# Kernel optimization log

Measured on AMD Instinct MI355X. Metric: run time of the kernel, lower is better.

## Reference

```python
import jax, jax.numpy as jnp
import numpy as np

DIM = 2            # dimension along which stripes are dropped (1=time, 2=freq)
DROP_WIDTH = 64    # max stripe width
STRIPES_NUM = 2    # stripes per sample


def setup_inputs() -> dict:
    key = jax.random.key(0)
    k1, k2, k3 = jax.random.split(key, 3)
    x = jax.random.normal(k1, (64, 2048, 512), dtype=jnp.float32)
    u_dist = jax.random.uniform(k2, (64, STRIPES_NUM), dtype=jnp.float32)
    u_bgn = jax.random.uniform(k3, (64, STRIPES_NUM), dtype=jnp.float32)
    return {"x": x, "u_dist": u_dist, "u_bgn": u_bgn}


def _keep_mask(u_dist, u_bgn, total_width):
    # distance ~ randint(0, drop_width); bgn ~ randint(0, total_width - distance)
    distance = jnp.floor(u_dist * DROP_WIDTH).astype(jnp.int32)          # [B, S]
    bgn = jnp.floor(u_bgn * (total_width - distance)).astype(jnp.int32)  # [B, S]
    idx = jnp.arange(total_width, dtype=jnp.int32)                        # [W]
    in_stripe = (idx[None, None, :] >= bgn[:, :, None]) & (
        idx[None, None, :] < (bgn + distance)[:, :, None]
    )  # [B, S, W]
    return ~jnp.any(in_stripe, axis=1)  # [B, W] True where values are kept


def reference(x, u_dist, u_bgn):
    total_width = x.shape[DIM]
    keep = _keep_mask(u_dist, u_bgn, total_width)  # [B, W]
    if DIM == 1:
        keep = keep[:, :, None]  # broadcast over freq bins
    else:
        keep = keep[:, None, :]  # broadcast over time steps
    return x * keep.astype(x.dtype)
```

## Files before the change

### kernel.cpp

```cpp
#include <hip/hip_runtime.h>


__global__ void DropStripes_kernel(const float4* __restrict__ x,
                                   const float* __restrict__ u_dist,
                                   const float* __restrict__ u_bgn,
                                   float4* __restrict__ out,
                                   int n4) {
    constexpr int W4 = 512 / 4;
    int idx = blockIdx.x * blockDim.x + threadIdx.x;
    int stride = gridDim.x * blockDim.x;
    for (int i = idx; i < n4; i += stride) {
        int b  = i >> 18;
        int c0 = (i & (W4 - 1)) << 2;

        float ud0 = u_dist[2 * b];
        float ud1 = u_dist[2 * b + 1];
        float ub0 = u_bgn[2 * b];
        float ub1 = u_bgn[2 * b + 1];

        int dist0 = (int)floorf(ud0 * 64.0f);
        int dist1 = (int)floorf(ud1 * 64.0f);
        int bgn0  = (int)floorf(ub0 * (float)(512 - dist0));
        int bgn1  = (int)floorf(ub1 * (float)(512 - dist1));
        int end0  = bgn0 + dist0;
        int end1  = bgn1 + dist1;

        float4 v = x[i];
        float* vp = reinterpret_cast<float*>(&v);
        #pragma unroll
        for (int j = 0; j < 4; ++j) {
            int c = c0 + j;
            bool drop = (c >= bgn0 && c < end0) || (c >= bgn1 && c < end1);
            vp[j] = drop ? 0.0f : vp[j];
        }
        out[i] = v;
    }
}

extern "C" void kernel_launch(void* const* d_in, const int* in_sizes, int n_in,
                              void* d_out, int out_size, void* d_ws, size_t ws_size,
                              hipStream_t stream) {
    const float* x      = (const float*)d_in[0];
    const float* u_dist = (const float*)d_in[1];
    const float* u_bgn  = (const float*)d_in[2];
    float* out          = (float*)d_out;

    int n4 = out_size / 4;
    int block = 256;
    int grid = 8192;
    DropStripes_kernel<<<grid, block, 0, stream>>>(
        (const float4*)x, u_dist, u_bgn, (float4*)out, n4);
}
```

Before: 102.3 us.

## Assign blocks per batch and hoist stripe mask out of unrolled loop

Each block now handles a contiguous chunk inside one batch. The per-batch stripe bounds and the per-thread column mask are computed once instead of on every grid-stride iteration, and the fixed 8-iteration loop is fully unrolled so several loads can be in flight per thread. This removes repeated scalar loads and index math from a memory-bound streaming kernel. Shapes are now hard-coded, and because the mask is applied by multiplication, NaN or Inf inputs inside a stripe produce NaN instead of zero.

```diff
diff --git a/kernel.cpp b/kernel.cpp
--- a/kernel.cpp
+++ b/kernel.cpp
@@ -1,38 +1,52 @@
 #include <hip/hip_runtime.h>
 
 
-__global__ void DropStripes_kernel(const float4* __restrict__ x,
-                                   const float* __restrict__ u_dist,
-                                   const float* __restrict__ u_bgn,
-                                   float4* __restrict__ out,
-                                   int n4) {
+typedef float f32x4 __attribute__((ext_vector_type(4)));
+
+__global__ void __launch_bounds__(256)
+DropStripes_kernel(const f32x4* __restrict__ x,
+                   const float* __restrict__ u_dist,
+                   const float* __restrict__ u_bgn,
+                   f32x4* __restrict__ out) {
     constexpr int W4 = 512 / 4;
-    int idx = blockIdx.x * blockDim.x + threadIdx.x;
-    int stride = gridDim.x * blockDim.x;
-    for (int i = idx; i < n4; i += stride) {
-        int b  = i >> 18;
-        int c0 = (i & (W4 - 1)) << 2;
+    constexpr int N4_PER_BATCH = 2048 * 512 / 4;
+    constexpr int BLOCKS_PER_BATCH = 128;
+    constexpr int CHUNK = N4_PER_BATCH / BLOCKS_PER_BATCH;
+    constexpr int ITERS = CHUNK / 256;
 
-        float ud0 = u_dist[2 * b];
-        float ud1 = u_dist[2 * b + 1];
-        float ub0 = u_bgn[2 * b];
-        float ub1 = u_bgn[2 * b + 1];
+    int b     = blockIdx.x >> 7;
+    int chunk = blockIdx.x & (BLOCKS_PER_BATCH - 1);
+    int base  = b * N4_PER_BATCH + chunk * CHUNK + (int)threadIdx.x;
 
-        int dist0 = (int)floorf(ud0 * 64.0f);
-        int dist1 = (int)floorf(ud1 * 64.0f);
-        int bgn0  = (int)floorf(ub0 * (float)(512 - dist0));
-        int bgn1  = (int)floorf(ub1 * (float)(512 - dist1));
-        int end0  = bgn0 + dist0;
-        int end1  = bgn1 + dist1;
+    float ud0 = u_dist[2 * b];
+    float ud1 = u_dist[2 * b + 1];
+    float ub0 = u_bgn[2 * b];
+    float ub1 = u_bgn[2 * b + 1];
 
-        float4 v = x[i];
-        float* vp = reinterpret_cast<float*>(&v);
-        #pragma unroll
-        for (int j = 0; j < 4; ++j) {
-            int c = c0 + j;
-            bool drop = (c >= bgn0 && c < end0) || (c >= bgn1 && c < end1);
-            vp[j] = drop ? 0.0f : vp[j];
-        }
+    int dist0 = (int)floorf(ud0 * 64.0f);
+    int dist1 = (int)floorf(ud1 * 64.0f);
+    int bgn0  = (int)floorf(ub0 * (float)(512 - dist0));
+    int bgn1  = (int)floorf(ub1 * (float)(512 - dist1));
+    int end0  = bgn0 + dist0;
+    int end1  = bgn1 + dist1;
+
+    int c0 = (base & (W4 - 1)) << 2;
+    float m[4];
+    #pragma unroll
+    for (int j = 0; j < 4; ++j) {
+        int c = c0 + j;
+        bool drop = (c >= bgn0 && c < end0) || (c >= bgn1 && c < end1);
+        m[j] = drop ? 0.0f : 1.0f;
+    }
+
+    #pragma unroll
+    for (int it = 0; it < ITERS; ++it) {
+        int i = base + it * 256;
+        f32x4 v = x[i];
+        v[0] *= m[0];
+        v[1] *= m[1];
+        v[2] *= m[2];
+        v[3] *= m[3];
         out[i] = v;
     }
 }
@@ -45,9 +59,7 @@
     const float* u_bgn  = (const float*)d_in[2];
     float* out          = (float*)d_out;
 
-    int n4 = out_size / 4;
-    int block = 256;
-    int grid = 8192;
-    DropStripes_kernel<<<grid, block, 0, stream>>>(
-        (const float4*)x, u_dist, u_bgn, (float4*)out, n4);
+    int grid = 64 * 128;
+    DropStripes_kernel<<<grid, 256, 0, stream>>>(
+        (const f32x4*)x, u_dist, u_bgn, (f32x4*)out);
 }
```

Result: faster. 100.3 us (-2.0%).
